# Kernel optimization log

Measured on AMD Instinct MI355X. Metric: run time of the kernel, lower is better.

## Reference

```python
import jax, jax.numpy as jnp
import numpy as np

EPS = 0.0001
N, E, DIN, H, DH, C, G = 50000, 800000, 256, 4, 64, 10, 100


def setup_inputs() -> dict:
    key = jax.random.key(0)
    ks = jax.random.split(key, 10)
    x = jax.random.normal(ks[0], (N, DIN), dtype=jnp.float32)
    src = jax.random.randint(ks[1], (E,), 0, N)
    dst = jax.random.randint(ks[2], (E,), 0, N)
    midx = jnp.stack([src, dst]).astype(jnp.int32)
    batch = jnp.sort(jax.random.randint(ks[3], (N,), 0, G)).astype(jnp.int32)
    W_feat = jax.random.normal(ks[4], (DIN, H * DH), dtype=jnp.float32) / np.sqrt(DIN)
    phi = jax.random.normal(ks[5], (H, 2 * DH, 1), dtype=jnp.float32) / np.sqrt(2 * DH)
    W1 = jax.random.normal(ks[6], (H * DH, DH), dtype=jnp.float32) / np.sqrt(H * DH)
    b1 = jnp.zeros((DH,), jnp.float32)
    W2 = jax.random.normal(ks[7], (DH, C), dtype=jnp.float32) / np.sqrt(DH)
    b2 = jnp.zeros((C,), jnp.float32)
    return {"x": x, "midx": midx, "batch": batch, "W_feat": W_feat,
            "phi": phi, "W1": W1, "b1": b1, "W2": W2, "b2": b2}


def reference(x, midx, batch, W_feat, phi, W1, b1, W2, b2):
    src, dst = midx[0], midx[1]
    # per-head node features [N, H, DH]
    h = (x @ W_feat).reshape(-1, H, DH)
    # concat-then-matmul with phi == sum of two half projections (GAT trick)
    phi_s = phi[:, :DH, 0]   # [H, DH]
    phi_d = phi[:, DH:, 0]   # [H, DH]
    a_s = jnp.einsum('nhd,hd->nh', h, phi_s)  # [N, H]
    a_d = jnp.einsum('nhd,hd->nh', h, phi_d)
    w = jax.nn.sigmoid(jax.nn.leaky_relu(a_s[src] + a_d[dst]))  # [E, H]
    msg = (h[dst] * w[:, :, None]).reshape(src.shape[0], H * DH)  # [E, H*DH]
    agg = jax.ops.segment_sum(msg, src, num_segments=x.shape[0])  # scatter_add
    # MLP head (dropout is identity in eval mode)
    z = jax.nn.leaky_relu(agg @ W1 + b1) @ W2 + b2  # [N, C]
    tmp = jnp.exp(z - jnp.max(z, axis=-1, keepdims=True)) + EPS
    preds = tmp / jnp.sum(tmp, axis=-1, keepdims=True)
    # global mean pool over graphs
    sums = jax.ops.segment_sum(preds, batch, num_segments=G)
    cnts = jax.ops.segment_sum(jnp.ones((batch.shape[0],), preds.dtype), batch, num_segments=G)
    yp = sums / cnts[:, None]
    return jnp.log(yp), preds
```

## Files before the change

kernel.cpp:

```cpp
#include <hip/hip_runtime.h>
#include <hip/hip_bf16.h>
#include <cstdint>

#define NN   50000
#define EE   800000
#define DIN_ 256
#define HD_  256
#define DH_  64
#define NH_  4
#define NC_  10
#define NG_  100
#define EPS_ 1e-4f
#define SLOPE_ 0.01f
#define AROW 40
#define CAP_ 48
#define FROW 264

typedef unsigned short ushortT;
typedef __attribute__((ext_vector_type(8))) short short8;
typedef __attribute__((ext_vector_type(4))) float f32x4;

__device__ __forceinline__ float leaky(float x) { return x >= 0.f ? x : SLOPE_ * x; }
__device__ __forceinline__ float sigm(float x)  { return 1.f / (1.f + __expf(-x)); }
__device__ __forceinline__ float b2f(ushortT u) { return __uint_as_float(((unsigned)u) << 16); }
__device__ __forceinline__ ushortT f2b(float f) {
    unsigned u = __float_as_uint(f);
    u += 0x7fffu + ((u >> 16) & 1u);
    return (ushortT)(u >> 16);
}

__global__ void setup_kernel(int* cursor,
                             const float* __restrict__ W, ushortT* __restrict__ wt,
                             const float* __restrict__ W1, ushortT* __restrict__ w1t,
                             const int* __restrict__ batch, int* __restrict__ gstart) {
    int i = blockIdx.x * 256 + threadIdx.x;
    if (i < NN) {
        cursor[i] = 0;
        int b = batch[i];
        int bp = (i == 0) ? -1 : batch[i - 1];
        for (int g = bp + 1; g <= b; g++) gstart[g] = i;
        if (i == NN - 1) {
            for (int g = b + 1; g <= NG_; g++) gstart[g] = NN;
        }
    }
    if (i < DIN_ * HD_) {
        int k = i >> 8, n = i & 255;
        wt[n * DIN_ + k] = f2b(W[i]);
    }
    if (i < 256 * 64) {
        int k = i >> 6, o = i & 63;
        w1t[o * 256 + k] = f2b(W1[i]);
    }
}

__global__ __launch_bounds__(256) void gemm_attn(const float* __restrict__ x,
                                                 const ushortT* __restrict__ wt,
                                                 const float* __restrict__ phi,
                                                 ushortT* __restrict__ hbf,
                                                 float* __restrict__ a_s,
                                                 float* __restrict__ a_d) {
    __shared__ ushortT A_lds[128 * AROW];
    __shared__ ushortT B_lds[128 * AROW];
    const int tid  = threadIdx.x;
    const int wave = tid >> 6, lane = tid & 63;
    const int wm = wave >> 1, wn = wave & 1;
    const int row0 = blockIdx.x * 128;
    const int col0 = blockIdx.y * 128;
    const int q = lane >> 4, l16 = lane & 15;

    f32x4 acc[4][4];
#pragma unroll
    for (int i = 0; i < 4; i++)
#pragma unroll
        for (int j = 0; j < 4; j++) acc[i][j] = (f32x4){0.f, 0.f, 0.f, 0.f};

    const int lm  = tid >> 1;
    const int lko = (tid & 1) * 16;

    for (int k0 = 0; k0 < DIN_; k0 += 32) {
        __syncthreads();
        {
            int gr = row0 + lm;
            float4 a0 = make_float4(0.f,0.f,0.f,0.f), a1 = a0, a2 = a0, a3 = a0;
            if (gr < NN) {
                const float4* xp = (const float4*)(x + (size_t)gr * DIN_ + k0 + lko);
                a0 = xp[0]; a1 = xp[1]; a2 = xp[2]; a3 = xp[3];
            }
            ushortT* ap = &A_lds[lm * AROW + lko];
            *(ushort4*)(ap + 0)  = make_ushort4(f2b(a0.x), f2b(a0.y), f2b(a0.z), f2b(a0.w));
            *(ushort4*)(ap + 4)  = make_ushort4(f2b(a1.x), f2b(a1.y), f2b(a1.z), f2b(a1.w));
            *(ushort4*)(ap + 8)  = make_ushort4(f2b(a2.x), f2b(a2.y), f2b(a2.z), f2b(a2.w));
            *(ushort4*)(ap + 12) = make_ushort4(f2b(a3.x), f2b(a3.y), f2b(a3.z), f2b(a3.w));
        }
        {
            const uint4* wp = (const uint4*)(wt + (size_t)(col0 + lm) * DIN_ + k0 + lko);
            uint4 b0 = wp[0], b1 = wp[1];
            *(uint4*)&B_lds[lm * AROW + lko + 0] = b0;
            *(uint4*)&B_lds[lm * AROW + lko + 8] = b1;
        }
        __syncthreads();

        short8 af[4], bf[4];
#pragma unroll
        for (int mi = 0; mi < 4; mi++)
            af[mi] = *(const short8*)&A_lds[(wm * 64 + mi * 16 + l16) * AROW + q * 8];
#pragma unroll
        for (int ni = 0; ni < 4; ni++)
            bf[ni] = *(const short8*)&B_lds[(wn * 64 + ni * 16 + l16) * AROW + q * 8];
#pragma unroll
        for (int mi = 0; mi < 4; mi++)
#pragma unroll
            for (int ni = 0; ni < 4; ni++)
                acc[mi][ni] = __builtin_amdgcn_mfma_f32_16x16x32_bf16(af[mi], bf[ni], acc[mi][ni], 0, 0, 0);
    }

#pragma unroll
    for (int mi = 0; mi < 4; mi++) {
        int rbase = row0 + wm * 64 + mi * 16 + q * 4;
#pragma unroll
        for (int ni = 0; ni < 4; ni++) {
            int c = col0 + wn * 64 + ni * 16 + l16;
#pragma unroll
            for (int r = 0; r < 4; r++) {
                int gr = rbase + r;
                if (gr < NN) hbf[(size_t)gr * HD_ + c] = f2b(acc[mi][ni][r]);
            }
        }
    }

    int head = blockIdx.y * 2 + wn;
    float phs[4], phd[4];
#pragma unroll
    for (int ni = 0; ni < 4; ni++) {
        phs[ni] = phi[head * 128 + ni * 16 + l16];
        phd[ni] = phi[head * 128 + 64 + ni * 16 + l16];
    }
#pragma unroll
    for (int mi = 0; mi < 4; mi++) {
#pragma unroll
        for (int r = 0; r < 4; r++) {
            float ps = acc[mi][0][r] * phs[0] + acc[mi][1][r] * phs[1]
                     + acc[mi][2][r] * phs[2] + acc[mi][3][r] * phs[3];
            float pd = acc[mi][0][r] * phd[0] + acc[mi][1][r] * phd[1]
                     + acc[mi][2][r] * phd[2] + acc[mi][3][r] * phd[3];
#pragma unroll
            for (int o = 1; o < 16; o <<= 1) {
                ps += __shfl_xor(ps, o);
                pd += __shfl_xor(pd, o);
            }
            if (l16 == 0) {
                int gr = row0 + wm * 64 + mi * 16 + q * 4 + r;
                if (gr < NN) {
                    a_s[gr * 4 + head] = ps;
                    a_d[gr * 4 + head] = pd;
                }
            }
        }
    }
}

__global__ void fill_edges(const int* __restrict__ src, const int* __restrict__ dstA,
                           int* __restrict__ cursor,
                           const float* __restrict__ a_s, const float* __restrict__ a_d,
                           uint4* __restrict__ edges) {
    int e = blockIdx.x * 256 + threadIdx.x;
    if (e >= EE) return;
    int s = src[e], d = dstA[e];
    int slot = atomicAdd(&cursor[s], 1);
    if (slot >= CAP_) return;
    float4 as4 = *(const float4*)(a_s + (size_t)s * 4);
    float4 ad4 = *(const float4*)(a_d + (size_t)d * 4);
    unsigned w01 = (unsigned)f2b(sigm(leaky(as4.x + ad4.x)))
                 | ((unsigned)f2b(sigm(leaky(as4.y + ad4.y))) << 16);
    unsigned w23 = (unsigned)f2b(sigm(leaky(as4.z + ad4.z)))
                 | ((unsigned)f2b(sigm(leaky(as4.w + ad4.w))) << 16);
    edges[(size_t)s * CAP_ + slot] = make_uint4((unsigned)d, w01, w23, 0u);
}

__global__ __launch_bounds__(256) void agg_mlp(const ushortT* __restrict__ hbf,
                                               const int* __restrict__ cursor,
                                               const uint4* __restrict__ edges,
                                               const ushortT* __restrict__ w1t,
                                               const float* __restrict__ b1,
                                               const float* __restrict__ W2,
                                               const float* __restrict__ b2,
                                               float* __restrict__ out) {
    union ShMem {
        uint4   E[16 * CAP_];
        ushortT A[16 * FROW];
    };
    __shared__ ShMem sh;
    __shared__ float z1t[16][68];
    __shared__ int   pcnt[16];
    const int tid = threadIdx.x;
    const int wave = tid >> 6, lane = tid & 63;
    const int q = lane >> 4, l16 = lane & 15;
    const int hsel = lane >> 4;
    const int wsh = (hsel & 1) * 16;
    const int n0 = blockIdx.x * 16;
    const ushortT* hrow = hbf + (size_t)lane * 4;

#pragma unroll
    for (int ii = 0; ii < 4; ii++) {
        int ln = wave * 4 + ii;
        int n = n0 + ln;
        int cnt = cursor[n];
        if (cnt > CAP_) cnt = CAP_;
        int pad = (cnt + 7) & ~7;
        if (lane == 0) pcnt[ln] = pad;
        if (lane < pad) {
            uint4 r = make_uint4(0u, 0u, 0u, 0u);
            if (lane < cnt) r = edges[(size_t)n * CAP_ + lane];
            sh.E[ln * CAP_ + lane] = r;
        }
    }
    __syncthreads();

    ushort4 o4v[4];
#pragma unroll
    for (int ii = 0; ii < 4; ii++) {
        int ln = wave * 4 + ii;
        int pc = pcnt[ln];
        const uint4* er = &sh.E[ln * CAP_];
        f32x4 acc = (f32x4){0.f, 0.f, 0.f, 0.f};
#pragma unroll 1
        for (int i = 0; i < pc; i += 8) {
            unsigned off[8]; float ww[8];
#pragma unroll
            for (int j = 0; j < 8; j++) {
                uint4 e = er[i + j];
                unsigned pair = (hsel & 2) ? e.z : e.y;
                ww[j] = b2f((ushortT)((pair >> wsh) & 0xffffu));
                off[j] = e.x * (unsigned)(HD_ * 2);
            }
            ushort4 hh[8];
#pragma unroll
            for (int j = 0; j < 8; j++)
                hh[j] = *(const ushort4*)((const char*)hrow + off[j]);
#pragma unroll
            for (int j = 0; j < 8; j++) {
                acc.x += b2f(hh[j].x) * ww[j];
                acc.y += b2f(hh[j].y) * ww[j];
                acc.z += b2f(hh[j].z) * ww[j];
                acc.w += b2f(hh[j].w) * ww[j];
            }
        }
        o4v[ii] = make_ushort4(f2b(acc.x), f2b(acc.y), f2b(acc.z), f2b(acc.w));
    }
    __syncthreads();

#pragma unroll
    for (int ii = 0; ii < 4; ii++) {
        int ln = wave * 4 + ii;
        *(ushort4*)&sh.A[ln * FROW + lane * 4] = o4v[ii];
    }
    __syncthreads();

    f32x4 macc = (f32x4){0.f, 0.f, 0.f, 0.f};
#pragma unroll
    for (int k0 = 0; k0 < 256; k0 += 32) {
        short8 af = *(const short8*)&sh.A[l16 * FROW + k0 + q * 8];
        short8 bf = *(const short8*)(w1t + (size_t)(wave * 16 + l16) * 256 + k0 + q * 8);
        macc = __builtin_amdgcn_mfma_f32_16x16x32_bf16(af, bf, macc, 0, 0, 0);
    }
    {
        int o = wave * 16 + l16;
        float bb = b1[o];
#pragma unroll
        for (int r = 0; r < 4; r++)
            z1t[q * 4 + r][o] = leaky(macc[r] + bb);
    }
    __syncthreads();

    if (tid < 16) {
        int n = n0 + tid;
        float zc[NC_];
#pragma unroll
        for (int c = 0; c < NC_; c++) zc[c] = b2[c];
        for (int k = 0; k < 64; k += 4) {
            float4 z4 = *(const float4*)&z1t[tid][k];
#pragma unroll
            for (int j = 0; j < 4; j++) {
                float zv = (j == 0) ? z4.x : (j == 1) ? z4.y : (j == 2) ? z4.z : z4.w;
#pragma unroll
                for (int c = 0; c < NC_; c++) zc[c] += zv * W2[(k + j) * NC_ + c];
            }
        }
        float m = zc[0];
#pragma unroll
        for (int c = 1; c < NC_; c++) m = fmaxf(m, zc[c]);
        float ssum = 0.f;
#pragma unroll
        for (int c = 0; c < NC_; c++) { zc[c] = __expf(zc[c] - m) + EPS_; ssum += zc[c]; }
        float inv = 1.f / ssum;
#pragma unroll
        for (int c = 0; c < NC_; c++) out[1000 + (size_t)n * NC_ + c] = zc[c] * inv;
    }
}

__global__ __launch_bounds__(256) void group_mean(const float* __restrict__ preds,
                                                  const int* __restrict__ gstart,
                                                  float* __restrict__ out) {
    __shared__ float red[16][16];
    int g = blockIdx.x;
    int t = threadIdx.x;
    int c = t & 15, chunk = t >> 4;
    int gs = gstart[g], ge = gstart[g + 1];
    float s = 0.f;
    if (c < NC_) {
        for (int n = gs + chunk; n < ge; n += 16) s += preds[(size_t)n * NC_ + c];
    }
    red[chunk][c] = s;
    __syncthreads();
    if (t < NC_) {
        float tot = 0.f;
#pragma unroll
        for (int j = 0; j < 16; j++) tot += red[j][t];
        out[g * NC_ + t] = __logf(tot / (float)(ge - gs));
    }
}

extern "C" void kernel_launch(void* const* d_in, const int* in_sizes, int n_in,
                              void* d_out, int out_size, void* d_ws, size_t ws_size,
                              hipStream_t stream) {
    const float* x      = (const float*)d_in[0];
    const int*   midx   = (const int*)d_in[1];
    const int*   batch  = (const int*)d_in[2];
    const float* W_feat = (const float*)d_in[3];
    const float* phi    = (const float*)d_in[4];
    const float* W1     = (const float*)d_in[5];
    const float* b1     = (const float*)d_in[6];
    const float* W2     = (const float*)d_in[7];
    const float* b2     = (const float*)d_in[8];
    const int* src = midx;
    const int* dst = midx + EE;
    float* out = (float*)d_out;

    char* p = (char*)d_ws;
    auto alloc = [&](size_t bytes) { void* r = (void*)p; p += (bytes + 255) & ~(size_t)255; return r; };
    ushortT* hbf      = (ushortT*)alloc((size_t)NN * HD_ * 2);
    uint4*   edges    = (uint4*)alloc((size_t)NN * CAP_ * 16);
    ushortT* wt       = (ushortT*)alloc((size_t)DIN_ * HD_ * 2);
    ushortT* w1t      = (ushortT*)alloc((size_t)64 * 256 * 2);
    float*   a_s      = (float*)alloc((size_t)NN * 4 * 4);
    float*   a_d      = (float*)alloc((size_t)NN * 4 * 4);
    int*     cursor   = (int*)alloc((size_t)NN * 4);
    int*     gstart   = (int*)alloc((size_t)(NG_ + 1) * 4);

    setup_kernel<<<256, 256, 0, stream>>>(cursor, W_feat, wt, W1, w1t, batch, gstart);
    gemm_attn<<<dim3((NN + 127) / 128, 2), 256, 0, stream>>>(x, wt, phi, hbf, a_s, a_d);
    fill_edges<<<(EE + 255) / 256, 256, 0, stream>>>(src, dst, cursor, a_s, a_d, edges);
    agg_mlp<<<NN / 16, 256, 0, stream>>>(hbf, cursor, edges, w1t, b1, W2, b2, out);
    group_mean<<<NG_, 256, 0, stream>>>(out + 1000, gstart, out);
}
```

Before: 247.8 us.

## Widen GEMM tile to all columns and use MFMA for second MLP layer

The feature GEMM now uses 512-thread blocks covering all 256 output columns per 128-row tile, so each x row is read and converted to bf16 once instead of twice. The second MLP layer and softmax in agg_mlp move from a 16-thread scalar loop to one wave doing a bf16 MFMA against a padded transposed W2, with shuffle-based max and sum. This removes redundant x traffic and a serial tail, at the cost of extra bf16 rounding on the hidden activations and W2, and larger blocks with fewer of them.

```diff
diff --git a/kernel.cpp b/kernel.cpp
--- a/kernel.cpp
+++ b/kernel.cpp
@@ -15,6 +15,7 @@
 #define AROW 40
 #define CAP_ 48
 #define FROW 264
+#define ZROW 80
 
 typedef unsigned short ushortT;
 typedef __attribute__((ext_vector_type(8))) short short8;
@@ -32,6 +33,7 @@
 __global__ void setup_kernel(int* cursor,
                              const float* __restrict__ W, ushortT* __restrict__ wt,
                              const float* __restrict__ W1, ushortT* __restrict__ w1t,
+                             const float* __restrict__ W2, ushortT* __restrict__ w2t,
                              const int* __restrict__ batch, int* __restrict__ gstart) {
     int i = blockIdx.x * 256 + threadIdx.x;
     if (i < NN) {
@@ -51,21 +53,24 @@
         int k = i >> 6, o = i & 63;
         w1t[o * 256 + k] = f2b(W1[i]);
     }
-}
-
-__global__ __launch_bounds__(256) void gemm_attn(const float* __restrict__ x,
+    if (i < 16 * 64) {
+        int c = i >> 6, k = i & 63;
+        w2t[i] = (c < NC_) ? f2b(W2[k * NC_ + c]) : (ushortT)0;
+    }
+}
+
+__global__ __launch_bounds__(512) void gemm_attn(const float* __restrict__ x,
                                                  const ushortT* __restrict__ wt,
                                                  const float* __restrict__ phi,
                                                  ushortT* __restrict__ hbf,
                                                  float* __restrict__ a_s,
                                                  float* __restrict__ a_d) {
     __shared__ ushortT A_lds[128 * AROW];
-    __shared__ ushortT B_lds[128 * AROW];
+    __shared__ ushortT B_lds[256 * AROW];
     const int tid  = threadIdx.x;
     const int wave = tid >> 6, lane = tid & 63;
-    const int wm = wave >> 1, wn = wave & 1;
+    const int wm = wave >> 2, wn = wave & 3;
     const int row0 = blockIdx.x * 128;
-    const int col0 = blockIdx.y * 128;
     const int q = lane >> 4, l16 = lane & 15;
 
     f32x4 acc[4][4];
@@ -74,29 +79,29 @@
 #pragma unroll
         for (int j = 0; j < 4; j++) acc[i][j] = (f32x4){0.f, 0.f, 0.f, 0.f};
 
-    const int lm  = tid >> 1;
-    const int lko = (tid & 1) * 16;
+    const int alm = tid >> 2;
+    const int alo = (tid & 3) * 8;
+    const int blm = tid >> 1;
+    const int blo = (tid & 1) * 16;
 
     for (int k0 = 0; k0 < DIN_; k0 += 32) {
         __syncthreads();
         {
-            int gr = row0 + lm;
-            float4 a0 = make_float4(0.f,0.f,0.f,0.f), a1 = a0, a2 = a0, a3 = a0;
+            int gr = row0 + alm;
+            float4 a0 = make_float4(0.f,0.f,0.f,0.f), a1 = a0;
             if (gr < NN) {
-                const float4* xp = (const float4*)(x + (size_t)gr * DIN_ + k0 + lko);
-                a0 = xp[0]; a1 = xp[1]; a2 = xp[2]; a3 = xp[3];
-            }
-            ushortT* ap = &A_lds[lm * AROW + lko];
-            *(ushort4*)(ap + 0)  = make_ushort4(f2b(a0.x), f2b(a0.y), f2b(a0.z), f2b(a0.w));
-            *(ushort4*)(ap + 4)  = make_ushort4(f2b(a1.x), f2b(a1.y), f2b(a1.z), f2b(a1.w));
-            *(ushort4*)(ap + 8)  = make_ushort4(f2b(a2.x), f2b(a2.y), f2b(a2.z), f2b(a2.w));
-            *(ushort4*)(ap + 12) = make_ushort4(f2b(a3.x), f2b(a3.y), f2b(a3.z), f2b(a3.w));
+                const float4* xp = (const float4*)(x + (size_t)gr * DIN_ + k0 + alo);
+                a0 = xp[0]; a1 = xp[1];
+            }
+            ushortT* ap = &A_lds[alm * AROW + alo];
+            *(ushort4*)(ap + 0) = make_ushort4(f2b(a0.x), f2b(a0.y), f2b(a0.z), f2b(a0.w));
+            *(ushort4*)(ap + 4) = make_ushort4(f2b(a1.x), f2b(a1.y), f2b(a1.z), f2b(a1.w));
         }
         {
-            const uint4* wp = (const uint4*)(wt + (size_t)(col0 + lm) * DIN_ + k0 + lko);
+            const uint4* wp = (const uint4*)(wt + (size_t)blm * DIN_ + k0 + blo);
             uint4 b0 = wp[0], b1 = wp[1];
-            *(uint4*)&B_lds[lm * AROW + lko + 0] = b0;
-            *(uint4*)&B_lds[lm * AROW + lko + 8] = b1;
+            *(uint4*)&B_lds[blm * AROW + blo + 0] = b0;
+            *(uint4*)&B_lds[blm * AROW + blo + 8] = b1;
         }
         __syncthreads();
 
@@ -119,7 +124,7 @@
         int rbase = row0 + wm * 64 + mi * 16 + q * 4;
 #pragma unroll
         for (int ni = 0; ni < 4; ni++) {
-            int c = col0 + wn * 64 + ni * 16 + l16;
+            int c = wn * 64 + ni * 16 + l16;
 #pragma unroll
             for (int r = 0; r < 4; r++) {
                 int gr = rbase + r;
@@ -128,7 +133,7 @@
         }
     }
 
-    int head = blockIdx.y * 2 + wn;
+    const int head = wn;
     float phs[4], phd[4];
 #pragma unroll
     for (int ni = 0; ni < 4; ni++) {
@@ -182,7 +187,7 @@
                                                const uint4* __restrict__ edges,
                                                const ushortT* __restrict__ w1t,
                                                const float* __restrict__ b1,
-                                               const float* __restrict__ W2,
+                                               const ushortT* __restrict__ w2t,
                                                const float* __restrict__ b2,
                                                float* __restrict__ out) {
     union ShMem {
@@ -190,8 +195,8 @@
         ushortT A[16 * FROW];
     };
     __shared__ ShMem sh;
-    __shared__ float z1t[16][68];
-    __shared__ int   pcnt[16];
+    __shared__ ushortT z1b[16 * ZROW];
+    __shared__ int pcnt[16];
     const int tid = threadIdx.x;
     const int wave = tid >> 6, lane = tid & 63;
     const int q = lane >> 4, l16 = lane & 15;
@@ -268,33 +273,34 @@
         float bb = b1[o];
 #pragma unroll
         for (int r = 0; r < 4; r++)
-            z1t[q * 4 + r][o] = leaky(macc[r] + bb);
-    }
-    __syncthreads();
-
-    if (tid < 16) {
-        int n = n0 + tid;
-        float zc[NC_];
-#pragma unroll
-        for (int c = 0; c < NC_; c++) zc[c] = b2[c];
-        for (int k = 0; k < 64; k += 4) {
-            float4 z4 = *(const float4*)&z1t[tid][k];
-#pragma unroll
-            for (int j = 0; j < 4; j++) {
-                float zv = (j == 0) ? z4.x : (j == 1) ? z4.y : (j == 2) ? z4.z : z4.w;
-#pragma unroll
-                for (int c = 0; c < NC_; c++) zc[c] += zv * W2[(k + j) * NC_ + c];
-            }
-        }
-        float m = zc[0];
-#pragma unroll
-        for (int c = 1; c < NC_; c++) m = fmaxf(m, zc[c]);
-        float ssum = 0.f;
-#pragma unroll
-        for (int c = 0; c < NC_; c++) { zc[c] = __expf(zc[c] - m) + EPS_; ssum += zc[c]; }
-        float inv = 1.f / ssum;
-#pragma unroll
-        for (int c = 0; c < NC_; c++) out[1000 + (size_t)n * NC_ + c] = zc[c] * inv;
+            z1b[(q * 4 + r) * ZROW + o] = f2b(leaky(macc[r] + bb));
+    }
+    __syncthreads();
+
+    if (wave == 0) {
+        f32x4 z2 = (f32x4){0.f, 0.f, 0.f, 0.f};
+#pragma unroll
+        for (int k0 = 0; k0 < 64; k0 += 32) {
+            short8 af = *(const short8*)&z1b[l16 * ZROW + k0 + q * 8];
+            short8 bf = *(const short8*)(w2t + l16 * 64 + k0 + q * 8);
+            z2 = __builtin_amdgcn_mfma_f32_16x16x32_bf16(af, bf, z2, 0, 0, 0);
+        }
+        float bb = (l16 < NC_) ? b2[l16] : 0.f;
+#pragma unroll
+        for (int r = 0; r < 4; r++) {
+            float v = (l16 < NC_) ? (z2[r] + bb) : -1e30f;
+            float m = v;
+#pragma unroll
+            for (int o = 1; o < 16; o <<= 1) m = fmaxf(m, __shfl_xor(m, o));
+            float ev = (l16 < NC_) ? (__expf(v - m) + EPS_) : 0.f;
+            float s = ev;
+#pragma unroll
+            for (int o = 1; o < 16; o <<= 1) s += __shfl_xor(s, o);
+            if (l16 < NC_) {
+                int n = n0 + q * 4 + r;
+                out[1000 + (size_t)n * NC_ + l16] = ev / s;
+            }
+        }
     }
 }
 
@@ -342,14 +348,15 @@
     uint4*   edges    = (uint4*)alloc((size_t)NN * CAP_ * 16);
     ushortT* wt       = (ushortT*)alloc((size_t)DIN_ * HD_ * 2);
     ushortT* w1t      = (ushortT*)alloc((size_t)64 * 256 * 2);
+    ushortT* w2t      = (ushortT*)alloc((size_t)16 * 64 * 2);
     float*   a_s      = (float*)alloc((size_t)NN * 4 * 4);
     float*   a_d      = (float*)alloc((size_t)NN * 4 * 4);
     int*     cursor   = (int*)alloc((size_t)NN * 4);
     int*     gstart   = (int*)alloc((size_t)(NG_ + 1) * 4);
 
-    setup_kernel<<<256, 256, 0, stream>>>(cursor, W_feat, wt, W1, w1t, batch, gstart);
-    gemm_attn<<<dim3((NN + 127) / 128, 2), 256, 0, stream>>>(x, wt, phi, hbf, a_s, a_d);
+    setup_kernel<<<256, 256, 0, stream>>>(cursor, W_feat, wt, W1, w1t, W2, w2t, batch, gstart);
+    gemm_attn<<<(NN + 127) / 128, 512, 0, stream>>>(x, wt, phi, hbf, a_s, a_d);
     fill_edges<<<(EE + 255) / 256, 256, 0, stream>>>(src, dst, cursor, a_s, a_d, edges);
-    agg_mlp<<<NN / 16, 256, 0, stream>>>(hbf, cursor, edges, w1t, b1, W2, b2, out);
+    agg_mlp<<<NN / 16, 256, 0, stream>>>(hbf, cursor, edges, w1t, b1, w2t, b2, out);
     group_mean<<<NG_, 256, 0, stream>>>(out + 1000, gstart, out);
 }
```

Measured after the change: 246.0 us. No clear change (-0.7%).
